# Performance work log

Measured on AMD Instinct MI355X. Metric: run time of the kernel, lower is better.

Reference implementation:

```python
import jax, jax.numpy as jnp
import numpy as np

N_GRAPHS = 64   # number of graphs in the batch
H = 128         # hidden dim
L = 3           # num_conv_layers
OUT = 64        # out_feature


def setup_inputs() -> dict:
    key = jax.random.key(0)
    ks = jax.random.split(key, 12)
    N, E, R, C = 10000, 160000, 2, 2
    s = 1.0 / np.sqrt(H)
    inp = {
        'x': jax.random.normal(ks[0], (N, H), jnp.float32),
        'edge_attr': jax.random.normal(ks[1], (E, H), jnp.float32),
        'node_mask': jax.random.uniform(ks[2], (R, C, N, 1), jnp.float32),
        'bond_W': jax.random.normal(ks[3], (L, H, H), jnp.float32) * s,
        'bond_b': jnp.zeros((L, H), jnp.float32),
        'eps': jnp.zeros((L,), jnp.float32),
        'conv_W1': jax.random.normal(ks[4], (L, H, H), jnp.float32) * s,
        'conv_b1': jnp.zeros((L, H), jnp.float32),
        'conv_W2': jax.random.normal(ks[5], (L, H, H), jnp.float32) * s,
        'conv_b2': jnp.zeros((L, H), jnp.float32),
        'mlp_W1': jax.random.normal(ks[6], (H, H), jnp.float32) * s,
        'mlp_b1': jnp.zeros((H,), jnp.float32),
        'mlp_W2': jax.random.normal(ks[7], (H, OUT), jnp.float32) * s,
        'mlp_b2': jnp.zeros((OUT,), jnp.float32),
        'edge_index': jax.random.randint(ks[8], (2, E), 0, N),
        'batch': jnp.sort(jax.random.randint(ks[9], (N,), 0, N_GRAPHS)),
    }
    return inp


def reference(x, edge_attr, node_mask, bond_W, bond_b, eps,
              conv_W1, conv_b1, conv_W2, conv_b2,
              mlp_W1, mlp_b1, mlp_W2, mlp_b2,
              edge_index, batch):
    gelu = lambda v: jax.nn.gelu(v, approximate=False)  # torch exact gelu
    R, C, N, _ = node_mask.shape
    src, dst = edge_index[0], edge_index[1]
    # edge_mask[r,c,e] = node_mask[r,c,src[e]] * node_mask[r,c,dst[e]]
    edge_mask = node_mask[:, :, src, :] * node_mask[:, :, dst, :]  # [R,C,E,1]
    # replica-offset graph ids: [R*C*N]
    batch_full = jnp.tile(batch, R * C) + jnp.repeat(jnp.arange(R * C), N) * N_GRAPHS
    # x repeated over (R, C): [R,C,N,H]
    h = jnp.broadcast_to(x[None, None], (R, C, N, x.shape[-1]))
    for i in range(L):
        emb = edge_attr @ bond_W[i] + bond_b[i]                    # [E,H]
        msg = gelu(h[:, :, src, :] + emb[None, None]) * edge_mask  # [R,C,E,H]
        agg = jnp.zeros_like(h).at[:, :, dst, :].add(msg)          # scatter_sum
        out = (1.0 + eps[i]) * h + agg
        out = gelu(out @ conv_W1[i] + conv_b1[i]) @ conv_W2[i] + conv_b2[i]
        h = gelu(out)  # norm=Identity, dropout=0
    hf = h.reshape(-1, h.shape[-1])                               # [R*C*N,H]
    y = gelu(hf @ mlp_W1 + mlp_b1) @ mlp_W2 + mlp_b2              # [R*C*N,OUT]
    fm = node_mask.reshape(-1, 1)
    D = R * N_GRAPHS * C
    num = jax.ops.segment_sum(y * fm, batch_full, num_segments=D)
    den = jax.ops.segment_sum(fm, batch_full, num_segments=D)
    return num / jnp.maximum(den, 1e-12)
```

## Files before the change

kernel.cpp:

```cpp
#include <hip/hip_runtime.h>

constexpr int H    = 128;
constexpr int NN   = 10000;
constexpr int EE   = 160000;
constexpr int RCN  = 4;
constexpr int NG   = 64;
constexpr int OUTF = 64;
constexpr int DSEG = 256;

using short8 = __attribute__((ext_vector_type(8))) short;
using f32x4  = __attribute__((ext_vector_type(4))) float;

__device__ __forceinline__ float gelu_f(float x){
  float z  = x*0.70710678118654752440f;
  float az = fabsf(z);
  float t  = __builtin_amdgcn_rcpf(fmaf(az, 0.3275911f, 1.0f));
  float e  = __expf(-z*z);
  float poly = fmaf(fmaf(fmaf(fmaf(1.061405429f, t, -1.453152027f),
                              t, 1.421413741f),
                         t, -0.284496736f),
                    t, 0.254829592f) * t;
  float er = fmaf(-poly, e, 1.0f);
  er = copysignf(er, z);
  return 0.5f*x*(1.0f + er);
}

__device__ __forceinline__ void split2(float x, unsigned short& h, unsigned short& m){
  unsigned int u = __float_as_uint(x);
  unsigned int rh = u + 0x7FFF + ((u>>16)&1);
  h = (unsigned short)(rh>>16);
  float fh = __uint_as_float((unsigned int)h << 16);
  float r1 = x - fh;
  unsigned int u1 = __float_as_uint(r1);
  unsigned int rm = u1 + 0x7FFF + ((u1>>16)&1);
  m = (unsigned short)(rm>>16);
}

__device__ __forceinline__ unsigned short bf16rne(float x){
  unsigned int u = __float_as_uint(x);
  return (unsigned short)((u + 0x7FFF + ((u>>16)&1))>>16);
}
__device__ __forceinline__ float bf2f(unsigned short v){
  return __uint_as_float((unsigned int)v << 16);
}

__global__ void k_hist(const int* __restrict__ dst, int* __restrict__ cnt){
  int e = blockIdx.x*256 + threadIdx.x;
  if(e < EE) atomicAdd(&cnt[dst[e]], 1);
}

__global__ __launch_bounds__(1024) void k_scan(const int* __restrict__ cnt,
                                               int* __restrict__ rs, int* __restrict__ cur){
  __shared__ int part[1024];
  int t = threadIdx.x;
  const int CH = 10;
  int base = t*CH;
  int s = 0;
  #pragma unroll
  for(int j=0;j<CH;j++){ int i = base+j; if(i<NN) s += cnt[i]; }
  part[t] = s;
  __syncthreads();
  for(int off=1; off<1024; off<<=1){
    int v = (t>=off) ? part[t-off] : 0;
    __syncthreads();
    part[t] += v;
    __syncthreads();
  }
  int run = (t==0) ? 0 : part[t-1];
  #pragma unroll
  for(int j=0;j<CH;j++){
    int i = base+j;
    if(i<NN){ rs[i] = run; cur[i] = run; run += cnt[i]; }
  }
  if(t == 1023) rs[NN] = part[1023];
}

__global__ void k_fill(const int* __restrict__ dst,
                       int* __restrict__ cur, int* __restrict__ eid){
  int e = blockIdx.x*256 + threadIdx.x;
  if(e >= EE) return;
  int p = atomicAdd(&cur[dst[e]], 1);
  eid[p] = e;
}

__global__ __launch_bounds__(256) void k_sortcsr(const int* __restrict__ rs, int* __restrict__ eid,
                          const int* __restrict__ src, int* __restrict__ esrc){
  int wid  = (blockIdx.x*256 + threadIdx.x) >> 6;
  int lane = threadIdx.x & 63;
  if(wid >= NN) return;
  int jb = rs[wid], je = rs[wid+1];
  int deg = je - jb;
  if(deg <= 0) return;
  if(deg == 1){
    if(lane == 0) esrc[jb] = src[eid[jb]];
    return;
  }
  if(deg <= 64){
    int v = (lane < deg) ? eid[jb + lane] : 0x7FFFFFFF;
    #pragma unroll
    for(int k=2; k<=64; k<<=1){
      #pragma unroll
      for(int j=k>>1; j>0; j>>=1){
        int o = __shfl_xor(v, j, 64);
        bool desc  = (lane & k) != 0;
        bool lower = (lane & j) == 0;
        v = ((lower != desc) ? min(v,o) : max(v,o));
      }
    }
    if(lane < deg){
      eid[jb+lane]  = v;
      esrc[jb+lane] = src[v];
    }
  } else if(lane == 0){
    for(int j=jb+1; j<je; j++){
      int v = eid[j];
      int k = j-1;
      while(k >= jb && eid[k] > v){ eid[k+1] = eid[k]; k--; }
      eid[k+1] = v;
    }
    for(int j=jb; j<je; j++) esrc[j] = src[eid[j]];
  }
}

__global__ void k_gbounds(const int* __restrict__ batch, int* __restrict__ gs){
  int g = threadIdx.x;
  if(g > NG) return;
  if(g == NG){ gs[NG] = NN; return; }
  int lo = 0, hi = NN;
  while(lo < hi){
    int mid = (lo+hi)>>1;
    if(batch[mid] < g) lo = mid+1; else hi = mid;
  }
  gs[g] = lo;
}

__global__ void k_emaskp(const int* __restrict__ src, const int* __restrict__ dst,
                         const int* __restrict__ eid, const float* __restrict__ nm,
                         float4* __restrict__ em4p){
  int j = blockIdx.x*256 + threadIdx.x;
  if(j >= EE) return;
  int e = eid[j];
  int s = src[e], d = dst[e];
  float4 m;
  m.x = nm[0*NN+s]*nm[0*NN+d];
  m.y = nm[1*NN+s]*nm[1*NN+d];
  m.z = nm[2*NN+s]*nm[2*NN+d];
  m.w = nm[3*NN+s]*nm[3*NN+d];
  em4p[j] = m;
}

__global__ void k_splitW(const float* __restrict__ W, unsigned short* __restrict__ oh,
                         unsigned short* __restrict__ om, int nmat, int N){
  int tid = blockIdx.x*256 + threadIdx.x;
  int total = nmat*128*N;
  if(tid >= total) return;
  int mat = tid / (128*N);
  int rem = tid - mat*(128*N);
  int k = rem / N;
  int n = rem - k*N;
  int NF = N >> 4;
  int ks = k >> 5, kk = k & 31;
  int nf = n >> 4;
  int lane = (n & 15) + 16*((kk & 15) >> 2);
  int e = 4*(kk >> 4) + (kk & 3);
  size_t idx = (size_t)mat*128*N + ((size_t)(ks*NF + nf)*64 + lane)*8 + e;
  unsigned short hh, mm;
  split2(W[tid], hh, mm);
  oh[idx] = hh; om[idx] = mm;
}

__global__ void k_splitA(const float* __restrict__ A, const int* __restrict__ eid,
                         unsigned short* __restrict__ oh){
  int tid = blockIdx.x*256 + threadIdx.x;
  if(tid >= EE*32) return;
  int j = tid >> 5, kq = tid & 31;
  int k = kq*4;
  int rsrc = eid[j];
  float4 v = *(const float4*)&A[(size_t)rsrc*H + k];
  ushort4 hh;
  hh.x = bf16rne(v.x); hh.y = bf16rne(v.y);
  hh.z = bf16rne(v.z); hh.w = bf16rne(v.w);
  *(ushort4*)&oh[(size_t)j*H + k] = hh;
}

template<int NFO, bool A2, bool GELU, int OMODE>
__global__ __launch_bounds__(256) void k_sgemm(
    const unsigned short* __restrict__ Ah, const unsigned short* __restrict__ Am,
    const unsigned short* __restrict__ Wh, const unsigned short* __restrict__ Wm,
    const float* __restrict__ bias, float* __restrict__ Cf,
    unsigned short* __restrict__ Oh, unsigned short* __restrict__ Om, int nrows){
  int t = threadIdx.x;
  int w = t >> 6, lane = t & 63;
  int m15 = lane & 15, kg = lane >> 4;
  int rowbase = blockIdx.x*128;

  const int SMAX = 4*NFO - 1;
  auto ldW = [&](int s, short8* d){
    size_t widx = ((size_t)s*64 + lane)*8;
    d[0] = *(const short8*)&Wh[widx];
    d[1] = *(const short8*)&Wm[widx];
  };

  int arow[2];
  #pragma unroll
  for(int mf=0;mf<2;mf++){
    int r = rowbase + w*32 + mf*16 + m15;
    arow[mf] = (r < nrows) ? r : (nrows-1);
  }

  f32x4 acc[2][NFO];
  #pragma unroll
  for(int mf=0;mf<2;mf++)
    #pragma unroll
    for(int nf=0;nf<NFO;nf++) acc[mf][nf] = (f32x4){0.f,0.f,0.f,0.f};

  short8 cw[2], nw[2];
  ldW(0, cw);
  ldW(1 <= SMAX ? 1 : SMAX, nw);

  for(int ks=0;ks<4;ks++){
    short8 ah[2], am[2];
    #pragma unroll
    for(int mf=0;mf<2;mf++){
      size_t base = (size_t)arow[mf]*H + ks*32 + kg*4;
      ushort4 hlo = *(const ushort4*)&Ah[base];
      ushort4 hhi = *(const ushort4*)&Ah[base + 16];
      ah[mf] = (short8){(short)hlo.x,(short)hlo.y,(short)hlo.z,(short)hlo.w,
                        (short)hhi.x,(short)hhi.y,(short)hhi.z,(short)hhi.w};
      if(A2){
        ushort4 mlo = *(const ushort4*)&Am[base];
        ushort4 mhi = *(const ushort4*)&Am[base + 16];
        am[mf] = (short8){(short)mlo.x,(short)mlo.y,(short)mlo.z,(short)mlo.w,
                          (short)mhi.x,(short)mhi.y,(short)mhi.z,(short)mhi.w};
      }
    }
    #pragma unroll
    for(int nf=0;nf<NFO;nf++){
      int s = ks*NFO + nf;
      short8 pw[2];
      ldW(s+2 <= SMAX ? s+2 : SMAX, pw);
      #pragma unroll
      for(int mf=0;mf<2;mf++){
        acc[mf][nf] = __builtin_amdgcn_mfma_f32_16x16x32_bf16(ah[mf], cw[0], acc[mf][nf], 0,0,0);
        acc[mf][nf] = __builtin_amdgcn_mfma_f32_16x16x32_bf16(ah[mf], cw[1], acc[mf][nf], 0,0,0);
        if(A2)
          acc[mf][nf] = __builtin_amdgcn_mfma_f32_16x16x32_bf16(am[mf], cw[0], acc[mf][nf], 0,0,0);
      }
      cw[0]=nw[0]; cw[1]=nw[1];
      nw[0]=pw[0]; nw[1]=pw[1];
    }
  }
  #pragma unroll
  for(int mf=0;mf<2;mf++){
    #pragma unroll
    for(int nf=0;nf<NFO;nf++){
      int gcol = nf*16 + m15;
      float bv = bias[gcol];
      #pragma unroll
      for(int r=0;r<4;r++){
        int grow = rowbase + w*32 + mf*16 + kg*4 + r;
        if(grow >= nrows) continue;
        float v = acc[mf][nf][r] + bv;
        if(GELU) v = gelu_f(v);
        size_t idx = (size_t)grow*(NFO*16) + gcol;
        if(OMODE == 0) Cf[idx] = v;
        if(OMODE == 1){
          unsigned short hh, mm2;
          split2(v, hh, mm2);
          Oh[idx] = hh; Om[idx] = mm2;
        }
        if(OMODE == 2) Oh[idx] = bf16rne(v);
      }
    }
  }
}

template<int NFO2, bool G2, int OMODE>
__global__ __launch_bounds__(256) void k_fuse2(
    const unsigned short* __restrict__ Ah, const unsigned short* __restrict__ Am,
    const unsigned short* __restrict__ W1h, const unsigned short* __restrict__ W1m,
    const float* __restrict__ b1,
    const unsigned short* __restrict__ W2h, const unsigned short* __restrict__ W2m,
    const float* __restrict__ b2,
    float* __restrict__ Cf,
    unsigned short* __restrict__ Oh, unsigned short* __restrict__ Om, int nrows){
  __shared__ unsigned int Ul[4*32*132];
  int t = threadIdx.x;
  int w = t >> 6, lane = t & 63;
  int m15 = lane & 15, kg = lane >> 4;
  int rowbase = blockIdx.x*128;
  unsigned int* Uw = &Ul[w*32*132];

  int arow[2];
  #pragma unroll
  for(int mf=0;mf<2;mf++){
    int r = rowbase + w*32 + mf*16 + m15;
    arow[mf] = (r < nrows) ? r : (nrows-1);
  }

  {
    const int SMAX = 31;
    auto ldW = [&](int s, short8* d){
      size_t widx = ((size_t)s*64 + lane)*8;
      d[0] = *(const short8*)&W1h[widx];
      d[1] = *(const short8*)&W1m[widx];
    };
    f32x4 acc[2][8];
    #pragma unroll
    for(int mf=0;mf<2;mf++)
      #pragma unroll
      for(int nf=0;nf<8;nf++) acc[mf][nf] = (f32x4){0.f,0.f,0.f,0.f};
    short8 cw[2], nw[2];
    ldW(0, cw); ldW(1, nw);
    for(int ks=0;ks<4;ks++){
      short8 ah[2], am[2];
      #pragma unroll
      for(int mf=0;mf<2;mf++){
        size_t base = (size_t)arow[mf]*H + ks*32 + kg*4;
        ushort4 hlo = *(const ushort4*)&Ah[base];
        ushort4 hhi = *(const ushort4*)&Ah[base + 16];
        ushort4 mlo = *(const ushort4*)&Am[base];
        ushort4 mhi = *(const ushort4*)&Am[base + 16];
        ah[mf] = (short8){(short)hlo.x,(short)hlo.y,(short)hlo.z,(short)hlo.w,
                          (short)hhi.x,(short)hhi.y,(short)hhi.z,(short)hhi.w};
        am[mf] = (short8){(short)mlo.x,(short)mlo.y,(short)mlo.z,(short)mlo.w,
                          (short)mhi.x,(short)mhi.y,(short)mhi.z,(short)mhi.w};
      }
      #pragma unroll
      for(int nf=0;nf<8;nf++){
        int s = ks*8 + nf;
        short8 pw[2];
        ldW(s+2 <= SMAX ? s+2 : SMAX, pw);
        #pragma unroll
        for(int mf=0;mf<2;mf++){
          acc[mf][nf] = __builtin_amdgcn_mfma_f32_16x16x32_bf16(ah[mf], cw[0], acc[mf][nf], 0,0,0);
          acc[mf][nf] = __builtin_amdgcn_mfma_f32_16x16x32_bf16(ah[mf], cw[1], acc[mf][nf], 0,0,0);
          acc[mf][nf] = __builtin_amdgcn_mfma_f32_16x16x32_bf16(am[mf], cw[0], acc[mf][nf], 0,0,0);
        }
        cw[0]=nw[0]; cw[1]=nw[1];
        nw[0]=pw[0]; nw[1]=pw[1];
      }
    }
    #pragma unroll
    for(int mf=0;mf<2;mf++){
      #pragma unroll
      for(int nf=0;nf<8;nf++){
        float bv = b1[nf*16 + m15];
        #pragma unroll
        for(int r=0;r<4;r++){
          float v = gelu_f(acc[mf][nf][r] + bv);
          unsigned short hh, mm2;
          split2(v, hh, mm2);
          int wrow = mf*16 + kg*4 + r;
          Uw[wrow*132 + nf*16 + m15] = (unsigned)hh | ((unsigned)mm2 << 16);
        }
      }
    }
  }
  __syncthreads();

  {
    const int SMAX = 4*NFO2 - 1;
    auto ldW = [&](int s, short8* d){
      size_t widx = ((size_t)s*64 + lane)*8;
      d[0] = *(const short8*)&W2h[widx];
      d[1] = *(const short8*)&W2m[widx];
    };
    f32x4 acc[2][NFO2];
    #pragma unroll
    for(int mf=0;mf<2;mf++)
      #pragma unroll
      for(int nf=0;nf<NFO2;nf++) acc[mf][nf] = (f32x4){0.f,0.f,0.f,0.f};
    short8 cw[2], nw[2];
    ldW(0, cw); ldW(1 <= SMAX ? 1 : SMAX, nw);
    for(int ks=0;ks<4;ks++){
      short8 ah[2], am[2];
      #pragma unroll
      for(int mf=0;mf<2;mf++){
        const unsigned int* base = &Uw[(mf*16 + m15)*132 + ks*32 + kg*4];
        uint4 q0 = *(const uint4*)base;
        uint4 q1 = *(const uint4*)(base + 16);
        unsigned h0 = (q0.x & 0xFFFFu) | (q0.y << 16);
        unsigned h1 = (q0.z & 0xFFFFu) | (q0.w << 16);
        unsigned h2 = (q1.x & 0xFFFFu) | (q1.y << 16);
        unsigned h3 = (q1.z & 0xFFFFu) | (q1.w << 16);
        unsigned M0 = (q0.x >> 16) | (q0.y & 0xFFFF0000u);
        unsigned M1 = (q0.z >> 16) | (q0.w & 0xFFFF0000u);
        unsigned M2 = (q1.x >> 16) | (q1.y & 0xFFFF0000u);
        unsigned M3 = (q1.z >> 16) | (q1.w & 0xFFFF0000u);
        union { uint4 u; short8 s; } cvh, cvm;
        cvh.u = (uint4){h0,h1,h2,h3};
        cvm.u = (uint4){M0,M1,M2,M3};
        ah[mf] = cvh.s; am[mf] = cvm.s;
      }
      #pragma unroll
      for(int nf=0;nf<NFO2;nf++){
        int s = ks*NFO2 + nf;
        short8 pw[2];
        ldW(s+2 <= SMAX ? s+2 : SMAX, pw);
        #pragma unroll
        for(int mf=0;mf<2;mf++){
          acc[mf][nf] = __builtin_amdgcn_mfma_f32_16x16x32_bf16(ah[mf], cw[0], acc[mf][nf], 0,0,0);
          acc[mf][nf] = __builtin_amdgcn_mfma_f32_16x16x32_bf16(ah[mf], cw[1], acc[mf][nf], 0,0,0);
          acc[mf][nf] = __builtin_amdgcn_mfma_f32_16x16x32_bf16(am[mf], cw[0], acc[mf][nf], 0,0,0);
        }
        cw[0]=nw[0]; cw[1]=nw[1];
        nw[0]=pw[0]; nw[1]=pw[1];
      }
    }
    #pragma unroll
    for(int mf=0;mf<2;mf++){
      #pragma unroll
      for(int nf=0;nf<NFO2;nf++){
        int gcol = nf*16 + m15;
        float bv = b2[gcol];
        #pragma unroll
        for(int r=0;r<4;r++){
          int grow = rowbase + w*32 + mf*16 + kg*4 + r;
          if(grow >= nrows) continue;
          float v = acc[mf][nf][r] + bv;
          if(G2) v = gelu_f(v);
          size_t idx = (size_t)grow*(NFO2*16) + gcol;
          if(OMODE == 0) Cf[idx] = v;
          if(OMODE == 1){
            unsigned short hh, mm2;
            split2(v, hh, mm2);
            Oh[idx] = hh; Om[idx] = mm2;
          }
          if(OMODE == 2) Oh[idx] = bf16rne(v);
        }
      }
    }
  }
}

template<bool FIRST>
__global__ __launch_bounds__(256) void k_agg(const float* __restrict__ xin,
                       const unsigned short* __restrict__ hB,
                       const unsigned short* __restrict__ embB, const float4* __restrict__ em4p,
                       const int* __restrict__ rs, const int* __restrict__ esrc,
                       const float* __restrict__ epsp,
                       unsigned short* __restrict__ Th, unsigned short* __restrict__ Tm){
  int t = threadIdx.x;
  int w = t >> 6;
  int lane = t & 63;
  int half = lane >> 5;
  int l32 = lane & 31;
  int n = blockIdx.x*4 + w;
  int d0 = l32*4;
  int rc0 = half*2, rc1 = rc0+1;
  float4 acc0 = {0.f,0.f,0.f,0.f}, acc1 = {0.f,0.f,0.f,0.f};
  int jb = rs[n], je = rs[n+1];

  float4 evs[3], h0s[3], h1s[3];
  float  m0s[3], m1s[3];

  auto ld = [&](int j, int slot){
    int s = esrc[j];
    ushort4 e4 = *(const ushort4*)&embB[(size_t)j*H + d0];
    evs[slot].x = bf2f(e4.x); evs[slot].y = bf2f(e4.y);
    evs[slot].z = bf2f(e4.z); evs[slot].w = bf2f(e4.w);
    float4 m = em4p[j];
    m0s[slot] = half ? m.z : m.x;
    m1s[slot] = half ? m.w : m.y;
    if(FIRST){
      h0s[slot] = *(const float4*)&xin[(size_t)s*H + d0];
      h1s[slot] = h0s[slot];
    } else {
      ushort4 a = *(const ushort4*)&hB[((size_t)s*RCN + rc0)*H + d0];
      ushort4 b = *(const ushort4*)&hB[((size_t)s*RCN + rc1)*H + d0];
      h0s[slot].x = bf2f(a.x); h0s[slot].y = bf2f(a.y);
      h0s[slot].z = bf2f(a.z); h0s[slot].w = bf2f(a.w);
      h1s[slot].x = bf2f(b.x); h1s[slot].y = bf2f(b.y);
      h1s[slot].z = bf2f(b.z); h1s[slot].w = bf2f(b.w);
    }
  };

  if(jb < je){
    ld(jb, 0);
    if(jb+1 < je) ld(jb+1, 1);
    if(jb+2 < je) ld(jb+2, 2);
    for(int j=jb; j<je; j++){
      float4 ev0 = evs[0], h00 = h0s[0], h10 = h1s[0];
      float  m00 = m0s[0], m10 = m1s[0];
      evs[0]=evs[1]; h0s[0]=h0s[1]; h1s[0]=h1s[1]; m0s[0]=m0s[1]; m1s[0]=m1s[1];
      evs[1]=evs[2]; h0s[1]=h0s[2]; h1s[1]=h1s[2]; m0s[1]=m0s[2]; m1s[1]=m1s[2];
      if(j+3 < je) ld(j+3, 2);
      if(FIRST){
        float gx = gelu_f(h00.x+ev0.x);
        float gy = gelu_f(h00.y+ev0.y);
        float gz = gelu_f(h00.z+ev0.z);
        float gw = gelu_f(h00.w+ev0.w);
        acc0.x += gx*m00; acc0.y += gy*m00; acc0.z += gz*m00; acc0.w += gw*m00;
        acc1.x += gx*m10; acc1.y += gy*m10; acc1.z += gz*m10; acc1.w += gw*m10;
      } else {
        acc0.x += gelu_f(h00.x+ev0.x)*m00;
        acc0.y += gelu_f(h00.y+ev0.y)*m00;
        acc0.z += gelu_f(h00.z+ev0.z)*m00;
        acc0.w += gelu_f(h00.w+ev0.w)*m00;
        acc1.x += gelu_f(h10.x+ev0.x)*m10;
        acc1.y += gelu_f(h10.y+ev0.y)*m10;
        acc1.z += gelu_f(h10.z+ev0.z)*m10;
        acc1.w += gelu_f(h10.w+ev0.w)*m10;
      }
    }
  }
  float e1 = 1.0f + epsp[0];
  #pragma unroll
  for(int p=0;p<2;p++){
    int rc = p ? rc1 : rc0;
    float4 ac = p ? acc1 : acc0;
    float4 hv;
    if(FIRST){
      hv = *(const float4*)&xin[(size_t)n*H + d0];
    } else {
      ushort4 a = *(const ushort4*)&hB[((size_t)n*RCN + rc)*H + d0];
      hv.x = bf2f(a.x); hv.y = bf2f(a.y); hv.z = bf2f(a.z); hv.w = bf2f(a.w);
    }
    float4 o;
    o.x = e1*hv.x + ac.x; o.y = e1*hv.y + ac.y;
    o.z = e1*hv.z + ac.z; o.w = e1*hv.w + ac.w;
    int row = n*RCN + rc;
    ushort4 hh, mm;
    split2(o.x, hh.x, mm.x);
    split2(o.y, hh.y, mm.y);
    split2(o.z, hh.z, mm.z);
    split2(o.w, hh.w, mm.w);
    size_t idx = (size_t)row*H + d0;
    *(ushort4*)&Th[idx] = hh;
    *(ushort4*)&Tm[idx] = mm;
  }
}

__global__ __launch_bounds__(64) void k_pool(const float* __restrict__ y, const float* __restrict__ nm,
                       const int* __restrict__ gs, float* __restrict__ out){
  int seg = blockIdx.x;
  int rc = seg / NG;
  int g  = seg - rc*NG;
  int c  = threadIdx.x;
  int nb = gs[g], ne = gs[g+1];
  float num = 0.f, den = 0.f;
  for(int n=nb; n<ne; n++){
    float w = nm[rc*NN + n];
    num += y[((size_t)n*RCN + rc)*OUTF + c] * w;
    den += w;
  }
  out[seg*OUTF + c] = num / fmaxf(den, 1e-12f);
}

extern "C" void kernel_launch(void* const* d_in, const int* in_sizes, int n_in,
                              void* d_out, int out_size, void* d_ws, size_t ws_size,
                              hipStream_t stream){
  const float* x         = (const float*)d_in[0];
  const float* edge_attr = (const float*)d_in[1];
  const float* node_mask = (const float*)d_in[2];
  const float* bond_W    = (const float*)d_in[3];
  const float* bond_b    = (const float*)d_in[4];
  const float* epsv      = (const float*)d_in[5];
  const float* conv_W1   = (const float*)d_in[6];
  const float* conv_b1   = (const float*)d_in[7];
  const float* conv_W2   = (const float*)d_in[8];
  const float* conv_b2   = (const float*)d_in[9];
  const float* mlp_W1    = (const float*)d_in[10];
  const float* mlp_b1    = (const float*)d_in[11];
  const float* mlp_W2    = (const float*)d_in[12];
  const float* mlp_b2    = (const float*)d_in[13];
  const int*   eidx      = (const int*)d_in[14];
  const int*   batch     = (const int*)d_in[15];
  const int* srcp = eidx;
  const int* dstp = eidx + EE;

  char* p = (char*)d_ws;
  auto alloc = [&](size_t bytes)->char*{
    char* r = p; p += (bytes + 255) & ~size_t(255); return r;
  };
  unsigned short* hB = (unsigned short*)alloc((size_t)RCN*NN*H*2);
  unsigned short* embB = (unsigned short*)alloc((size_t)EE*H*2);
  float4* em4p = (float4*)alloc((size_t)EE*16);
  float*  y    = (float*) alloc((size_t)RCN*NN*OUTF*4);
  int*    cnt  = (int*)   alloc((size_t)NN*4);
  int*    rs   = (int*)   alloc((size_t)(NN+1)*4);
  int*    cur  = (int*)   alloc((size_t)NN*4);
  int*    eid  = (int*)   alloc((size_t)EE*4);
  int*    esrc = (int*)   alloc((size_t)EE*4);
  int*    gs   = (int*)   alloc((size_t)(NG+1)*4);
  unsigned short* WBh  = (unsigned short*)alloc((size_t)3*16384*2);
  unsigned short* WBm  = (unsigned short*)alloc((size_t)3*16384*2);
  unsigned short* WC1h = (unsigned short*)alloc((size_t)3*16384*2);
  unsigned short* WC1m = (unsigned short*)alloc((size_t)3*16384*2);
  unsigned short* WC2h = (unsigned short*)alloc((size_t)3*16384*2);
  unsigned short* WC2m = (unsigned short*)alloc((size_t)3*16384*2);
  unsigned short* WM1h = (unsigned short*)alloc((size_t)16384*2);
  unsigned short* WM1m = (unsigned short*)alloc((size_t)16384*2);
  unsigned short* WM2h = (unsigned short*)alloc((size_t)8192*2);
  unsigned short* WM2m = (unsigned short*)alloc((size_t)8192*2);
  unsigned short* EAh  = (unsigned short*)alloc((size_t)EE*H*2);
  const size_t NPB = (size_t)RCN*NN*H*2;
  unsigned short* TBh = (unsigned short*)alloc(NPB);
  unsigned short* TBm = (unsigned short*)alloc(NPB);
  if((size_t)(p - (char*)d_ws) > ws_size) return;

  hipMemsetAsync(cnt, 0, (size_t)NN*4, stream);

  k_hist    <<<(EE+255)/256, 256, 0, stream>>>(dstp, cnt);
  k_scan    <<<1, 1024, 0, stream>>>(cnt, rs, cur);
  k_fill    <<<(EE+255)/256, 256, 0, stream>>>(dstp, cur, eid);
  k_sortcsr <<<(NN*64+255)/256, 256, 0, stream>>>(rs, eid, srcp, esrc);
  k_emaskp  <<<(EE+255)/256, 256, 0, stream>>>(srcp, dstp, eid, node_mask, em4p);
  k_splitA  <<<EE*32/256, 256, 0, stream>>>(edge_attr, eid, EAh);
  k_gbounds <<<1, 128, 0, stream>>>(batch, gs);
  k_splitW  <<<192, 256, 0, stream>>>(bond_W,  WBh,  WBm,  3, 128);
  k_splitW  <<<192, 256, 0, stream>>>(conv_W1, WC1h, WC1m, 3, 128);
  k_splitW  <<<192, 256, 0, stream>>>(conv_W2, WC2h, WC2m, 3, 128);
  k_splitW  <<<64,  256, 0, stream>>>(mlp_W1,  WM1h, WM1m, 1, 128);
  k_splitW  <<<32,  256, 0, stream>>>(mlp_W2,  WM2h, WM2m, 1, 64);

  const int NROWS = RCN*NN;
  const int GB_E = EE/128;
  const int GB_N = (NROWS+127)/128;
  for(int l=0; l<3; l++){
    size_t wo = (size_t)l*16384;
    k_sgemm<8,false,false,2><<<GB_E, 256, 0, stream>>>(
        EAh, nullptr, WBh+wo, WBm+wo, bond_b + l*H, nullptr, embB, nullptr, EE);
    if(l == 0)
      k_agg<true ><<<NN/4, 256, 0, stream>>>(x, nullptr, embB, em4p, rs, esrc,
                                             epsv + l, TBh, TBm);
    else
      k_agg<false><<<NN/4, 256, 0, stream>>>(nullptr, hB, embB, em4p, rs, esrc,
                                             epsv + l, TBh, TBm);
    if(l < 2)
      k_fuse2<8,true,2><<<GB_N, 256, 0, stream>>>(
          TBh, TBm, WC1h+wo, WC1m+wo, conv_b1 + l*H,
          WC2h+wo, WC2m+wo, conv_b2 + l*H, nullptr, hB, nullptr, NROWS);
    else
      k_fuse2<8,true,1><<<GB_N, 256, 0, stream>>>(
          TBh, TBm, WC1h+wo, WC1m+wo, conv_b1 + l*H,
          WC2h+wo, WC2m+wo, conv_b2 + l*H, nullptr, TBh, TBm, NROWS);
  }
  k_fuse2<4,false,0><<<GB_N, 256, 0, stream>>>(
      TBh, TBm, WM1h, WM1m, mlp_b1, WM2h, WM2m, mlp_b2,
      y, nullptr, nullptr, NROWS);
  k_pool<<<DSEG, 64, 0, stream>>>(y, node_mask, gs, (float*)d_out);
}
```

Baseline: 571.9 us.

## Schedule aggregation nodes by descending degree and keep hidden state in fp32

Adds a counting sort of destination nodes by in-degree (histogram, scan, fill) so the aggregation kernel processes high-degree nodes first, which should reduce wave tail imbalance. The inter-layer hidden state is also stored as fp32 rather than bf16, which removes rounding error and conversion work but doubles the bytes gathered per edge. Node order in each block now depends on degree, so neighbouring waves no longer touch adjacent rows, and three small kernels plus a memset are added.

```diff
diff --git a/kernel.cpp b/kernel.cpp
--- a/kernel.cpp
+++ b/kernel.cpp
@@ -132,6 +132,28 @@
     if(batch[mid] < g) lo = mid+1; else hi = mid;
   }
   gs[g] = lo;
+}
+
+__global__ void k_dhist(const int* __restrict__ rs, int* __restrict__ dcnt){
+  int n = blockIdx.x*256 + threadIdx.x;
+  if(n >= NN) return;
+  int deg = rs[n+1] - rs[n];
+  if(deg > 255) deg = 255;
+  atomicAdd(&dcnt[deg], 1);
+}
+__global__ void k_dscan(const int* __restrict__ dcnt, int* __restrict__ dcur){
+  if(threadIdx.x != 0) return;
+  int run = 0;
+  for(int d = 255; d >= 0; d--){ dcur[d] = run; run += dcnt[d]; }
+}
+__global__ void k_dfill(const int* __restrict__ rs, int* __restrict__ dcur,
+                        int* __restrict__ nord){
+  int n = blockIdx.x*256 + threadIdx.x;
+  if(n >= NN) return;
+  int deg = rs[n+1] - rs[n];
+  if(deg > 255) deg = 255;
+  int p = atomicAdd(&dcur[deg], 1);
+  nord[p] = n;
 }
 
 __global__ void k_emaskp(const int* __restrict__ src, const int* __restrict__ dst,
@@ -435,10 +457,10 @@
 }
 
 template<bool FIRST>
-__global__ __launch_bounds__(256) void k_agg(const float* __restrict__ xin,
-                       const unsigned short* __restrict__ hB,
+__global__ __launch_bounds__(256) void k_agg(const float* __restrict__ hin,
                        const unsigned short* __restrict__ embB, const float4* __restrict__ em4p,
                        const int* __restrict__ rs, const int* __restrict__ esrc,
+                       const int* __restrict__ nord,
                        const float* __restrict__ epsp,
                        unsigned short* __restrict__ Th, unsigned short* __restrict__ Tm){
   int t = threadIdx.x;
@@ -446,7 +468,7 @@
   int lane = t & 63;
   int half = lane >> 5;
   int l32 = lane & 31;
-  int n = blockIdx.x*4 + w;
+  int n = nord[blockIdx.x*4 + w];
   int d0 = l32*4;
   int rc0 = half*2, rc1 = rc0+1;
   float4 acc0 = {0.f,0.f,0.f,0.f}, acc1 = {0.f,0.f,0.f,0.f};
@@ -464,15 +486,11 @@
     m0s[slot] = half ? m.z : m.x;
     m1s[slot] = half ? m.w : m.y;
     if(FIRST){
-      h0s[slot] = *(const float4*)&xin[(size_t)s*H + d0];
+      h0s[slot] = *(const float4*)&hin[(size_t)s*H + d0];
       h1s[slot] = h0s[slot];
     } else {
-      ushort4 a = *(const ushort4*)&hB[((size_t)s*RCN + rc0)*H + d0];
-      ushort4 b = *(const ushort4*)&hB[((size_t)s*RCN + rc1)*H + d0];
-      h0s[slot].x = bf2f(a.x); h0s[slot].y = bf2f(a.y);
-      h0s[slot].z = bf2f(a.z); h0s[slot].w = bf2f(a.w);
-      h1s[slot].x = bf2f(b.x); h1s[slot].y = bf2f(b.y);
-      h1s[slot].z = bf2f(b.z); h1s[slot].w = bf2f(b.w);
+      h0s[slot] = *(const float4*)&hin[((size_t)s*RCN + rc0)*H + d0];
+      h1s[slot] = *(const float4*)&hin[((size_t)s*RCN + rc1)*H + d0];
     }
   };
 
@@ -510,13 +528,8 @@
   for(int p=0;p<2;p++){
     int rc = p ? rc1 : rc0;
     float4 ac = p ? acc1 : acc0;
-    float4 hv;
-    if(FIRST){
-      hv = *(const float4*)&xin[(size_t)n*H + d0];
-    } else {
-      ushort4 a = *(const ushort4*)&hB[((size_t)n*RCN + rc)*H + d0];
-      hv.x = bf2f(a.x); hv.y = bf2f(a.y); hv.z = bf2f(a.z); hv.w = bf2f(a.w);
-    }
+    const float* hb = FIRST ? (hin + (size_t)n*H) : (hin + ((size_t)n*RCN + rc)*H);
+    float4 hv = *(const float4*)&hb[d0];
     float4 o;
     o.x = e1*hv.x + ac.x; o.y = e1*hv.y + ac.y;
     o.z = e1*hv.z + ac.z; o.w = e1*hv.w + ac.w;
@@ -574,7 +587,7 @@
   auto alloc = [&](size_t bytes)->char*{
     char* r = p; p += (bytes + 255) & ~size_t(255); return r;
   };
-  unsigned short* hB = (unsigned short*)alloc((size_t)RCN*NN*H*2);
+  float*  h    = (float*) alloc((size_t)RCN*NN*H*4);
   unsigned short* embB = (unsigned short*)alloc((size_t)EE*H*2);
   float4* em4p = (float4*)alloc((size_t)EE*16);
   float*  y    = (float*) alloc((size_t)RCN*NN*OUTF*4);
@@ -584,6 +597,9 @@
   int*    eid  = (int*)   alloc((size_t)EE*4);
   int*    esrc = (int*)   alloc((size_t)EE*4);
   int*    gs   = (int*)   alloc((size_t)(NG+1)*4);
+  int*    dcnt = (int*)   alloc((size_t)256*4);
+  int*    dcur = (int*)   alloc((size_t)256*4);
+  int*    nord = (int*)   alloc((size_t)NN*4);
   unsigned short* WBh  = (unsigned short*)alloc((size_t)3*16384*2);
   unsigned short* WBm  = (unsigned short*)alloc((size_t)3*16384*2);
   unsigned short* WC1h = (unsigned short*)alloc((size_t)3*16384*2);
@@ -601,11 +617,15 @@
   if((size_t)(p - (char*)d_ws) > ws_size) return;
 
   hipMemsetAsync(cnt, 0, (size_t)NN*4, stream);
+  hipMemsetAsync(dcnt, 0, (size_t)256*4, stream);
 
   k_hist    <<<(EE+255)/256, 256, 0, stream>>>(dstp, cnt);
   k_scan    <<<1, 1024, 0, stream>>>(cnt, rs, cur);
   k_fill    <<<(EE+255)/256, 256, 0, stream>>>(dstp, cur, eid);
   k_sortcsr <<<(NN*64+255)/256, 256, 0, stream>>>(rs, eid, srcp, esrc);
+  k_dhist   <<<(NN+255)/256, 256, 0, stream>>>(rs, dcnt);
+  k_dscan   <<<1, 64, 0, stream>>>(dcnt, dcur);
+  k_dfill   <<<(NN+255)/256, 256, 0, stream>>>(rs, dcur, nord);
   k_emaskp  <<<(EE+255)/256, 256, 0, stream>>>(srcp, dstp, eid, node_mask, em4p);
   k_splitA  <<<EE*32/256, 256, 0, stream>>>(edge_attr, eid, EAh);
   k_gbounds <<<1, 128, 0, stream>>>(batch, gs);
@@ -623,15 +643,15 @@
     k_sgemm<8,false,false,2><<<GB_E, 256, 0, stream>>>(
         EAh, nullptr, WBh+wo, WBm+wo, bond_b + l*H, nullptr, embB, nullptr, EE);
     if(l == 0)
-      k_agg<true ><<<NN/4, 256, 0, stream>>>(x, nullptr, embB, em4p, rs, esrc,
+      k_agg<true ><<<NN/4, 256, 0, stream>>>(x, embB, em4p, rs, esrc, nord,
                                              epsv + l, TBh, TBm);
     else
-      k_agg<false><<<NN/4, 256, 0, stream>>>(nullptr, hB, embB, em4p, rs, esrc,
+      k_agg<false><<<NN/4, 256, 0, stream>>>(h, embB, em4p, rs, esrc, nord,
                                              epsv + l, TBh, TBm);
     if(l < 2)
-      k_fuse2<8,true,2><<<GB_N, 256, 0, stream>>>(
+      k_fuse2<8,true,0><<<GB_N, 256, 0, stream>>>(
           TBh, TBm, WC1h+wo, WC1m+wo, conv_b1 + l*H,
-          WC2h+wo, WC2m+wo, conv_b2 + l*H, nullptr, hB, nullptr, NROWS);
+          WC2h+wo, WC2m+wo, conv_b2 + l*H, h, nullptr, nullptr, NROWS);
     else
       k_fuse2<8,true,1><<<GB_N, 256, 0, stream>>>(
           TBh, TBm, WC1h+wo, WC1m+wo, conv_b1 + l*H,
```

Measured after the change: 584.2 us. +2.1%, slower.
